# Optimization experiments

Hardware: AMD Instinct MI355X
Metric: run time of the kernel (lower is better)

## Reference

```python
import jax, jax.numpy as jnp
import numpy as np

N_NODES = 50000
N_EDGES = 800000
N_GRAPHS = 512
VOCAB = 100000
EMB = 64
HID = 128
CLASSES = 2


def setup_inputs() -> dict:
    key = jax.random.key(0)
    ks = jax.random.split(key, 12)
    x = jax.random.randint(ks[0], (N_NODES,), 0, VOCAB)
    edge_index = jax.random.randint(ks[1], (2, N_EDGES), 0, N_NODES)
    batch = jnp.sort(jax.random.randint(ks[2], (N_NODES,), 0, N_GRAPHS))
    s = lambda fan_in: 1.0 / np.sqrt(fan_in)
    emb_table = jax.random.normal(ks[3], (VOCAB, EMB), jnp.float32)
    w1_l = jax.random.uniform(ks[4], (EMB, HID), jnp.float32, -s(EMB), s(EMB))
    b1 = jnp.zeros((HID,), jnp.float32)
    w1_r = jax.random.uniform(ks[5], (EMB, HID), jnp.float32, -s(EMB), s(EMB))
    w2_l = jax.random.uniform(ks[6], (HID, HID), jnp.float32, -s(HID), s(HID))
    b2 = jnp.zeros((HID,), jnp.float32)
    w2_r = jax.random.uniform(ks[7], (HID, HID), jnp.float32, -s(HID), s(HID))
    w_out = jax.random.uniform(ks[8], (HID, CLASSES), jnp.float32, -s(HID), s(HID))
    b_out = jnp.zeros((CLASSES,), jnp.float32)
    return {"x": x, "edge_index": edge_index, "batch": batch,
            "emb_table": emb_table, "w1_l": w1_l, "b1": b1, "w1_r": w1_r,
            "w2_l": w2_l, "b2": b2, "w2_r": w2_r, "w_out": w_out, "b_out": b_out}


def _sage_conv(h, src, dst, w_l, b_l, w_r):
    # PyG SAGEConv (mean aggr): out = lin_l(mean_{j in N(i)} x_j) + lin_r(x_i)
    msg = h[src]                                              # [E, F] gather
    agg = jax.ops.segment_sum(msg, dst, num_segments=N_NODES)  # [N, F]
    deg = jax.ops.segment_sum(jnp.ones((src.shape[0],), h.dtype), dst,
                              num_segments=N_NODES)
    mean = agg / jnp.maximum(deg, 1.0)[:, None]
    return mean @ w_l + b_l + h @ w_r


def reference(x, edge_index, batch, emb_table, w1_l, b1, w1_r,
              w2_l, b2, w2_r, w_out, b_out):
    src, dst = edge_index[0], edge_index[1]
    h = emb_table[x]                                          # [N, EMB]
    h = jax.nn.relu(_sage_conv(h, src, dst, w1_l, b1, w1_r))
    # dropout is identity in eval mode
    h = jax.nn.relu(_sage_conv(h, src, dst, w2_l, b2, w2_r))
    # global mean pool over graphs
    pooled = jax.ops.segment_sum(h, batch, num_segments=N_GRAPHS)
    cnt = jax.ops.segment_sum(jnp.ones((N_NODES,), h.dtype), batch,
                              num_segments=N_GRAPHS)
    pooled = pooled / jnp.maximum(cnt, 1.0)[:, None]
    return pooled @ w_out + b_out                              # [G, CLASSES]
```

## Files before the change

kernel.cpp:

```cpp
#include <hip/hip_runtime.h>
#include <hip/hip_bf16.h>

#define N_NODES 50000
#define N_EDGES 800000
#define N_GRAPHS 512
#define EMB 64
#define HID 128

__device__ __forceinline__ unsigned f2bf(float f) {
    unsigned x = __float_as_uint(f);
    return (x + 0x7fffu + ((x >> 16) & 1u)) >> 16;
}
__device__ __forceinline__ unsigned packbf(float lo, float hi) {
    return f2bf(lo) | (f2bf(hi) << 16);
}
__device__ __forceinline__ float bf_lo(unsigned u) { return __uint_as_float(u << 16); }
__device__ __forceinline__ float bf_hi(unsigned u) { return __uint_as_float(u & 0xffff0000u); }

__global__ void k_embed_hist(const int* __restrict__ x, const float* __restrict__ emb,
                             const int* __restrict__ ei, uint2* __restrict__ h0b,
                             int* __restrict__ deg) {
    int t = blockIdx.x * 256 + threadIdx.x;
    if (t >= N_EDGES) return;
    int n = t >> 4, c4 = t & 15;
    const float4* e4 = (const float4*)emb;
    float4 v = e4[(size_t)x[n] * 16 + c4];
    uint2 b; b.x = packbf(v.x, v.y); b.y = packbf(v.z, v.w);
    h0b[(size_t)n * 16 + c4] = b;
    atomicAdd(&deg[ei[N_EDGES + t]], 1);
}

__global__ void k_scanA(const int* __restrict__ deg, int* __restrict__ rowptr,
                        int* __restrict__ bsums) {
    __shared__ int s[256];
    int t = threadIdx.x, i = blockIdx.x * 256 + t;
    int v = (i < N_NODES) ? deg[i] : 0;
    s[t] = v; __syncthreads();
    int xv = v;
    for (int off = 1; off < 256; off <<= 1) {
        int y = (t >= off) ? s[t - off] : 0;
        __syncthreads();
        xv += y; s[t] = xv;
        __syncthreads();
    }
    if (i < N_NODES) rowptr[i] = xv - v;
    if (t == 255) bsums[blockIdx.x] = xv;
}

__global__ void k_scanB(int* __restrict__ bsums, int nb) {
    __shared__ int s[256];
    int t = threadIdx.x;
    int v = (t < nb) ? bsums[t] : 0;
    s[t] = v; __syncthreads();
    int xv = v;
    for (int off = 1; off < 256; off <<= 1) {
        int y = (t >= off) ? s[t - off] : 0;
        __syncthreads();
        xv += y; s[t] = xv;
        __syncthreads();
    }
    if (t < nb) bsums[t] = xv - v;
}

__global__ void k_scanC(int* __restrict__ rowptr, int* __restrict__ wp,
                        const int* __restrict__ bsums) {
    int i = blockIdx.x * 256 + threadIdx.x;
    if (i < N_NODES) {
        int v = rowptr[i] + bsums[blockIdx.x];
        rowptr[i] = v;
        wp[i] = v;
    }
    if (i == 0) rowptr[N_NODES] = N_EDGES;
}

__global__ void k_scatter(const int* __restrict__ ei, int* __restrict__ wp,
                          int* __restrict__ nbr) {
    int e = blockIdx.x * 256 + threadIdx.x;
    if (e >= N_EDGES) return;
    int s = ei[e], d = ei[N_EDGES + e];
    int pos = atomicAdd(&wp[d], 1);
    nbr[pos] = s;
}

template <int F>
__device__ __forceinline__ void agg_tile_bf(const uint2* __restrict__ hb,
                                            const int* __restrict__ rowptr,
                                            const int* __restrict__ nbr,
                                            float* __restrict__ mean,
                                            int aggIdx, int t) {
    int wl = t >> 6;
    int l = t & 63;
    float4* m4 = (float4*)mean;

    int n, c;
    if constexpr (F == 128) { n = aggIdx * 16 + wl * 2 + (l >> 5); c = l & 31; }
    else                    { n = aggIdx * 32 + wl * 4 + (l >> 4); c = l & 15; }
    if (n >= N_NODES) return;
    constexpr int CU2 = F / 4;

    int r0 = rowptr[n], r1 = rowptr[n + 1];
    float inv = 1.0f / (float)max(r1 - r0, 1);

    float4 a[8];
    #pragma unroll
    for (int u = 0; u < 8; ++u) a[u] = make_float4(0.f, 0.f, 0.f, 0.f);

    int i = r0;
    for (; i + 7 < r1; i += 8) {
        int s0 = nbr[i + 0], s1 = nbr[i + 1], s2 = nbr[i + 2], s3 = nbr[i + 3];
        int s4 = nbr[i + 4], s5 = nbr[i + 5], s6 = nbr[i + 6], s7 = nbr[i + 7];
        uint2 v0 = hb[(size_t)s0 * CU2 + c];
        uint2 v1 = hb[(size_t)s1 * CU2 + c];
        uint2 v2 = hb[(size_t)s2 * CU2 + c];
        uint2 v3 = hb[(size_t)s3 * CU2 + c];
        uint2 v4 = hb[(size_t)s4 * CU2 + c];
        uint2 v5 = hb[(size_t)s5 * CU2 + c];
        uint2 v6 = hb[(size_t)s6 * CU2 + c];
        uint2 v7 = hb[(size_t)s7 * CU2 + c];
        a[0].x += bf_lo(v0.x); a[0].y += bf_hi(v0.x); a[0].z += bf_lo(v0.y); a[0].w += bf_hi(v0.y);
        a[1].x += bf_lo(v1.x); a[1].y += bf_hi(v1.x); a[1].z += bf_lo(v1.y); a[1].w += bf_hi(v1.y);
        a[2].x += bf_lo(v2.x); a[2].y += bf_hi(v2.x); a[2].z += bf_lo(v2.y); a[2].w += bf_hi(v2.y);
        a[3].x += bf_lo(v3.x); a[3].y += bf_hi(v3.x); a[3].z += bf_lo(v3.y); a[3].w += bf_hi(v3.y);
        a[4].x += bf_lo(v4.x); a[4].y += bf_hi(v4.x); a[4].z += bf_lo(v4.y); a[4].w += bf_hi(v4.y);
        a[5].x += bf_lo(v5.x); a[5].y += bf_hi(v5.x); a[5].z += bf_lo(v5.y); a[5].w += bf_hi(v5.y);
        a[6].x += bf_lo(v6.x); a[6].y += bf_hi(v6.x); a[6].z += bf_lo(v6.y); a[6].w += bf_hi(v6.y);
        a[7].x += bf_lo(v7.x); a[7].y += bf_hi(v7.x); a[7].z += bf_lo(v7.y); a[7].w += bf_hi(v7.y);
    }
    for (; i + 3 < r1; i += 4) {
        int s0 = nbr[i + 0], s1 = nbr[i + 1], s2 = nbr[i + 2], s3 = nbr[i + 3];
        uint2 v0 = hb[(size_t)s0 * CU2 + c];
        uint2 v1 = hb[(size_t)s1 * CU2 + c];
        uint2 v2 = hb[(size_t)s2 * CU2 + c];
        uint2 v3 = hb[(size_t)s3 * CU2 + c];
        a[0].x += bf_lo(v0.x); a[0].y += bf_hi(v0.x); a[0].z += bf_lo(v0.y); a[0].w += bf_hi(v0.y);
        a[1].x += bf_lo(v1.x); a[1].y += bf_hi(v1.x); a[1].z += bf_lo(v1.y); a[1].w += bf_hi(v1.y);
        a[2].x += bf_lo(v2.x); a[2].y += bf_hi(v2.x); a[2].z += bf_lo(v2.y); a[2].w += bf_hi(v2.y);
        a[3].x += bf_lo(v3.x); a[3].y += bf_hi(v3.x); a[3].z += bf_lo(v3.y); a[3].w += bf_hi(v3.y);
    }
    for (; i < r1; ++i) {
        uint2 v = hb[(size_t)nbr[i] * CU2 + c];
        a[0].x += bf_lo(v.x); a[0].y += bf_hi(v.x); a[0].z += bf_lo(v.y); a[0].w += bf_hi(v.y);
    }
    #pragma unroll
    for (int u = 1; u < 8; ++u) {
        a[0].x += a[u].x; a[0].y += a[u].y; a[0].z += a[u].z; a[0].w += a[u].w;
    }
    m4[(size_t)n * CU2 + c] = make_float4(a[0].x * inv, a[0].y * inv,
                                          a[0].z * inv, a[0].w * inv);
}

template <int K>
__device__ __forceinline__ void stage_f32(const float* __restrict__ hin, int base,
                                          int t, float* ls) {
    constexpr int LS = K + 2, C4 = K / 4;
    const float4* h4 = (const float4*)hin;
    for (int idx = t; idx < 64 * C4; idx += 512) {
        int r = idx / C4, c = idx % C4;
        float4 v = (base + r < N_NODES) ? h4[(size_t)(base + r) * C4 + c]
                                        : make_float4(0.f, 0.f, 0.f, 0.f);
        float* dp = &ls[r * LS + c * 4];
        dp[0] = v.x; dp[1] = v.y; dp[2] = v.z; dp[3] = v.w;
    }
}

template <int K>
__device__ __forceinline__ void stage_bf(const uint2* __restrict__ hb, int base,
                                         int t, float* ls) {
    constexpr int LS = K + 2, C2 = K / 4;
    for (int idx = t; idx < 64 * C2; idx += 512) {
        int r = idx / C2, c = idx % C2;
        uint2 v = (base + r < N_NODES) ? hb[(size_t)(base + r) * C2 + c]
                                       : make_uint2(0u, 0u);
        float* dp = &ls[r * LS + c * 4];
        dp[0] = bf_lo(v.x); dp[1] = bf_hi(v.x);
        dp[2] = bf_lo(v.y); dp[3] = bf_hi(v.y);
    }
}

template <int K>
__device__ __forceinline__ void gemm_core(const float* __restrict__ lrow,
                                          const float* __restrict__ w,
                                          int j0, float (&acc)[16]) {
    #pragma unroll 4
    for (int k = 0; k < K; ++k) {
        float hv = lrow[k];
        const float* wk = &w[(size_t)k * 128 + j0];
        #pragma unroll
        for (int j = 0; j < 16; ++j) acc[j] = fmaf(hv, wk[j], acc[j]);
    }
}

__global__ __launch_bounds__(512) void k_fuse1(
    const uint2* __restrict__ h0b, const int* __restrict__ rowptr,
    const int* __restrict__ nbr, float* __restrict__ mean1,
    const float* __restrict__ w1r, const float* __restrict__ b1,
    float* __restrict__ pre1) {
    __shared__ float ls[64 * 66];
    int b = blockIdx.x, t = threadIdx.x;
    if (b % 3 == 2) {
        int base = (b / 3) * 64;
        stage_bf<64>(h0b, base, t, ls);
        __syncthreads();
        int lane = t & 63, wid = __builtin_amdgcn_readfirstlane(t >> 6), j0 = wid * 16;
        int node = base + lane;
        float acc[16];
        #pragma unroll
        for (int j = 0; j < 16; ++j) acc[j] = b1[j0 + j];
        gemm_core<64>(&ls[lane * 66], w1r, j0, acc);
        if (node < N_NODES) {
            float4* o4 = (float4*)pre1;
            #pragma unroll
            for (int jj = 0; jj < 4; ++jj)
                o4[(size_t)node * 32 + wid * 4 + jj] =
                    make_float4(acc[jj*4], acc[jj*4+1], acc[jj*4+2], acc[jj*4+3]);
        }
    } else {
        agg_tile_bf<64>(h0b, rowptr, nbr, mean1, (b / 3) * 2 + (b % 3), t);
    }
}

__global__ __launch_bounds__(512) void k_fuse2(
    const uint2* __restrict__ h1b, const int* __restrict__ rowptr,
    const int* __restrict__ nbr, float* __restrict__ mean2,
    const float* __restrict__ w2r, const float* __restrict__ b2,
    float* __restrict__ pre2) {
    __shared__ float ls[64 * 130];
    int b = blockIdx.x, t = threadIdx.x;
    if (b % 5 == 4) {
        int base = (b / 5) * 64;
        stage_bf<128>(h1b, base, t, ls);
        __syncthreads();
        int lane = t & 63, wid = __builtin_amdgcn_readfirstlane(t >> 6), j0 = wid * 16;
        int node = base + lane;
        float acc[16];
        #pragma unroll
        for (int j = 0; j < 16; ++j) acc[j] = b2[j0 + j];
        gemm_core<128>(&ls[lane * 130], w2r, j0, acc);
        if (node < N_NODES) {
            float4* o4 = (float4*)pre2;
            #pragma unroll
            for (int jj = 0; jj < 4; ++jj)
                o4[(size_t)node * 32 + wid * 4 + jj] =
                    make_float4(acc[jj*4], acc[jj*4+1], acc[jj*4+2], acc[jj*4+3]);
        }
    } else {
        agg_tile_bf<128>(h1b, rowptr, nbr, mean2, (b / 5) * 4 + (b % 5), t);
    }
}

__global__ __launch_bounds__(512) void k_gemm_mean64(
    const float* __restrict__ mean1, const float* __restrict__ w1l,
    const float* __restrict__ pre1, uint2* __restrict__ h1b) {
    __shared__ float ls[64 * 66];
    int t = threadIdx.x, base = blockIdx.x * 64;
    stage_f32<64>(mean1, base, t, ls);
    __syncthreads();
    int lane = t & 63, wid = __builtin_amdgcn_readfirstlane(t >> 6), j0 = wid * 16;
    int node = base + lane;
    bool valid = node < N_NODES;
    float acc[16];
    const float4* p4 = (const float4*)pre1;
    #pragma unroll
    for (int jj = 0; jj < 4; ++jj) {
        float4 v = valid ? p4[(size_t)node * 32 + wid * 4 + jj]
                         : make_float4(0.f, 0.f, 0.f, 0.f);
        acc[jj*4] = v.x; acc[jj*4+1] = v.y; acc[jj*4+2] = v.z; acc[jj*4+3] = v.w;
    }
    gemm_core<64>(&ls[lane * 66], w1l, j0, acc);
    if (!valid) return;
    #pragma unroll
    for (int jj = 0; jj < 4; ++jj) {
        float a0 = fmaxf(acc[jj*4+0], 0.f), a1 = fmaxf(acc[jj*4+1], 0.f);
        float a2 = fmaxf(acc[jj*4+2], 0.f), a3 = fmaxf(acc[jj*4+3], 0.f);
        uint2 u; u.x = packbf(a0, a1); u.y = packbf(a2, a3);
        h1b[(size_t)node * 32 + wid * 4 + jj] = u;
    }
}

__global__ __launch_bounds__(512) void k_mean128_pool(
    const float* __restrict__ mean2, const float* __restrict__ w2l,
    const float* __restrict__ pre2, const int* __restrict__ batch,
    float* __restrict__ pooled) {
    __shared__ float ls[64 * 130];
    __shared__ int bb[64];
    int t = threadIdx.x, base = blockIdx.x * 64;
    stage_f32<128>(mean2, base, t, ls);
    if (t < 64) bb[t] = (base + t < N_NODES) ? batch[base + t] : -1;
    __syncthreads();
    int lane = t & 63, wid = __builtin_amdgcn_readfirstlane(t >> 6), j0 = wid * 16;
    int node = base + lane;
    bool valid = node < N_NODES;
    float acc[16];
    const float4* p4 = (const float4*)pre2;
    #pragma unroll
    for (int jj = 0; jj < 4; ++jj) {
        float4 v = valid ? p4[(size_t)node * 32 + wid * 4 + jj]
                         : make_float4(0.f, 0.f, 0.f, 0.f);
        acc[jj*4] = v.x; acc[jj*4+1] = v.y; acc[jj*4+2] = v.z; acc[jj*4+3] = v.w;
    }
    gemm_core<128>(&ls[lane * 130], w2l, j0, acc);
    __syncthreads();
    #pragma unroll
    for (int j = 0; j < 16; ++j)
        ls[lane * 129 + j0 + j] = valid ? fmaxf(acc[j], 0.f) : 0.f;
    __syncthreads();
    if (t < 128) {
        int col = t;
        float run = 0.f;
        int gcur = bb[0];
        for (int r = 0; r < 64; ++r) {
            int g = bb[r];
            if (g != gcur) {
                if (gcur >= 0) atomicAdd(&pooled[gcur * 128 + col], run);
                run = 0.f; gcur = g;
            }
            run += ls[r * 129 + col];
        }
        if (gcur >= 0) atomicAdd(&pooled[gcur * 128 + col], run);
    }
}

__global__ void k_head(const float* __restrict__ pooled, const int* __restrict__ batch,
                       const float* __restrict__ w_out, const float* __restrict__ b_out,
                       float* __restrict__ out) {
    int g = blockIdx.x, f = threadIdx.x;
    int lo = 0, hi = N_NODES;
    while (lo < hi) { int m = (lo + hi) >> 1; if (batch[m] < g) lo = m + 1; else hi = m; }
    int s = lo;
    lo = s; hi = N_NODES;
    while (lo < hi) { int m = (lo + hi) >> 1; if (batch[m] < g + 1) lo = m + 1; else hi = m; }
    int cnt = lo - s;
    float p = pooled[(size_t)g * 128 + f] / (float)max(cnt, 1);
    __shared__ float red[256];
    red[f] = p * w_out[f * 2 + 0];
    red[128 + f] = p * w_out[f * 2 + 1];
    __syncthreads();
    for (int st = 64; st > 0; st >>= 1) {
        if (f < st) { red[f] += red[f + st]; red[128 + f] += red[128 + f + st]; }
        __syncthreads();
    }
    if (f == 0) {
        out[(size_t)g * 2 + 0] = red[0] + b_out[0];
        out[(size_t)g * 2 + 1] = red[128] + b_out[1];
    }
}

extern "C" void kernel_launch(void* const* d_in, const int* in_sizes, int n_in,
                              void* d_out, int out_size, void* d_ws, size_t ws_size,
                              hipStream_t stream) {
    const int*   x      = (const int*)d_in[0];
    const int*   ei     = (const int*)d_in[1];
    const int*   batch  = (const int*)d_in[2];
    const float* emb    = (const float*)d_in[3];
    const float* w1_l   = (const float*)d_in[4];
    const float* b1     = (const float*)d_in[5];
    const float* w1_r   = (const float*)d_in[6];
    const float* w2_l   = (const float*)d_in[7];
    const float* b2     = (const float*)d_in[8];
    const float* w2_r   = (const float*)d_in[9];
    const float* w_out  = (const float*)d_in[10];
    const float* b_out  = (const float*)d_in[11];
    float* out = (float*)d_out;

    float* F = (float*)d_ws;
    float* mean1 = F;
    uint2* h1b   = (uint2*)F;
    float* pre1  = F + (size_t)N_NODES * 64;
    float* pre2  = pre1;
    float* mean2 = pre1 + (size_t)N_NODES * 128;
    uint2* h0b   = (uint2*)(mean2 + (size_t)N_NODES * 128);
    int*   deg   = (int*)((float*)h0b + (size_t)N_NODES * 32);
    float* pooled= (float*)(deg + N_NODES);
    int*   rowptr= (int*)(pooled + (size_t)N_GRAPHS * 128);
    int*   wp    = rowptr + N_NODES + 1;
    int*   nbr   = wp + N_NODES;
    int*   bsums = nbr + N_EDGES;

    const int NB = (N_NODES + 255) / 256;
    const int GB = (N_NODES + 63) / 64;

    hipMemsetAsync(deg, 0, (size_t)N_NODES * sizeof(int)
                          + (size_t)N_GRAPHS * 128 * sizeof(float), stream);

    k_embed_hist<<<(N_EDGES + 255) / 256, 256, 0, stream>>>(x, emb, ei, h0b, deg);
    k_scanA<<<NB, 256, 0, stream>>>(deg, rowptr, bsums);
    k_scanB<<<1, 256, 0, stream>>>(bsums, NB);
    k_scanC<<<NB, 256, 0, stream>>>(rowptr, wp, bsums);
    k_scatter<<<(N_EDGES + 255) / 256, 256, 0, stream>>>(ei, wp, nbr);

    k_fuse1<<<3 * GB, 512, 0, stream>>>(h0b, rowptr, nbr, mean1, w1_r, b1, pre1);
    k_gemm_mean64<<<GB, 512, 0, stream>>>(mean1, w1_l, pre1, h1b);

    k_fuse2<<<5 * GB, 512, 0, stream>>>(h1b, rowptr, nbr, mean2, w2_r, b2, pre2);
    k_mean128_pool<<<GB, 512, 0, stream>>>(mean2, w2_l, pre2, batch, pooled);

    k_head<<<N_GRAPHS, 128, 0, stream>>>(pooled, batch, w_out, b_out, out);

    (void)in_sizes; (void)n_in; (void)out_size; (void)ws_size;
}
```

Measured before the change: 332.8 us.

## Fuse neighbor aggregation and both linear transforms into one kernel per layer

Each SAGE layer now runs as a single kernel per 64-node tile. The kernel aggregates the neighbor mean straight into LDS, stages the self features as packed bf16, and computes both matmuls plus ReLU (and pooling for layer 2) without writing mean or pre-activation arrays to global memory. This removes two kernel launches and the fp32 global round-trips of mean1/mean2/pre1/pre2. The trade-off is fewer, heavier blocks with more LDS per block, where gather latency and GEMM are now serialized within a block instead of spread over separate blocks, which may reduce parallelism and latency hiding.

```diff
diff --git a/kernel.cpp b/kernel.cpp
--- a/kernel.cpp
+++ b/kernel.cpp
@@ -4,8 +4,6 @@
 #define N_NODES 50000
 #define N_EDGES 800000
 #define N_GRAPHS 512
-#define EMB 64
-#define HID 128
 
 __device__ __forceinline__ unsigned f2bf(float f) {
     unsigned x = __float_as_uint(f);
@@ -83,227 +81,175 @@
 }
 
 template <int F>
-__device__ __forceinline__ void agg_tile_bf(const uint2* __restrict__ hb,
-                                            const int* __restrict__ rowptr,
-                                            const int* __restrict__ nbr,
-                                            float* __restrict__ mean,
-                                            int aggIdx, int t) {
-    int wl = t >> 6;
-    int l = t & 63;
-    float4* m4 = (float4*)mean;
-
-    int n, c;
-    if constexpr (F == 128) { n = aggIdx * 16 + wl * 2 + (l >> 5); c = l & 31; }
-    else                    { n = aggIdx * 32 + wl * 4 + (l >> 4); c = l & 15; }
-    if (n >= N_NODES) return;
+__device__ __forceinline__ void agg_to_lds(const uint2* __restrict__ hb,
+                                           const int* __restrict__ rowptr,
+                                           const int* __restrict__ nbr,
+                                           int base, int pass, int t,
+                                           float* __restrict__ tB) {
     constexpr int CU2 = F / 4;
-
-    int r0 = rowptr[n], r1 = rowptr[n + 1];
-    float inv = 1.0f / (float)max(r1 - r0, 1);
-
-    float4 a[8];
-    #pragma unroll
-    for (int u = 0; u < 8; ++u) a[u] = make_float4(0.f, 0.f, 0.f, 0.f);
-
-    int i = r0;
-    for (; i + 7 < r1; i += 8) {
-        int s0 = nbr[i + 0], s1 = nbr[i + 1], s2 = nbr[i + 2], s3 = nbr[i + 3];
-        int s4 = nbr[i + 4], s5 = nbr[i + 5], s6 = nbr[i + 6], s7 = nbr[i + 7];
-        uint2 v0 = hb[(size_t)s0 * CU2 + c];
-        uint2 v1 = hb[(size_t)s1 * CU2 + c];
-        uint2 v2 = hb[(size_t)s2 * CU2 + c];
-        uint2 v3 = hb[(size_t)s3 * CU2 + c];
-        uint2 v4 = hb[(size_t)s4 * CU2 + c];
-        uint2 v5 = hb[(size_t)s5 * CU2 + c];
-        uint2 v6 = hb[(size_t)s6 * CU2 + c];
-        uint2 v7 = hb[(size_t)s7 * CU2 + c];
-        a[0].x += bf_lo(v0.x); a[0].y += bf_hi(v0.x); a[0].z += bf_lo(v0.y); a[0].w += bf_hi(v0.y);
-        a[1].x += bf_lo(v1.x); a[1].y += bf_hi(v1.x); a[1].z += bf_lo(v1.y); a[1].w += bf_hi(v1.y);
-        a[2].x += bf_lo(v2.x); a[2].y += bf_hi(v2.x); a[2].z += bf_lo(v2.y); a[2].w += bf_hi(v2.y);
-        a[3].x += bf_lo(v3.x); a[3].y += bf_hi(v3.x); a[3].z += bf_lo(v3.y); a[3].w += bf_hi(v3.y);
-        a[4].x += bf_lo(v4.x); a[4].y += bf_hi(v4.x); a[4].z += bf_lo(v4.y); a[4].w += bf_hi(v4.y);
-        a[5].x += bf_lo(v5.x); a[5].y += bf_hi(v5.x); a[5].z += bf_lo(v5.y); a[5].w += bf_hi(v5.y);
-        a[6].x += bf_lo(v6.x); a[6].y += bf_hi(v6.x); a[6].z += bf_lo(v6.y); a[6].w += bf_hi(v6.y);
-        a[7].x += bf_lo(v7.x); a[7].y += bf_hi(v7.x); a[7].z += bf_lo(v7.y); a[7].w += bf_hi(v7.y);
-    }
-    for (; i + 3 < r1; i += 4) {
-        int s0 = nbr[i + 0], s1 = nbr[i + 1], s2 = nbr[i + 2], s3 = nbr[i + 3];
-        uint2 v0 = hb[(size_t)s0 * CU2 + c];
-        uint2 v1 = hb[(size_t)s1 * CU2 + c];
-        uint2 v2 = hb[(size_t)s2 * CU2 + c];
-        uint2 v3 = hb[(size_t)s3 * CU2 + c];
-        a[0].x += bf_lo(v0.x); a[0].y += bf_hi(v0.x); a[0].z += bf_lo(v0.y); a[0].w += bf_hi(v0.y);
-        a[1].x += bf_lo(v1.x); a[1].y += bf_hi(v1.x); a[1].z += bf_lo(v1.y); a[1].w += bf_hi(v1.y);
-        a[2].x += bf_lo(v2.x); a[2].y += bf_hi(v2.x); a[2].z += bf_lo(v2.y); a[2].w += bf_hi(v2.y);
-        a[3].x += bf_lo(v3.x); a[3].y += bf_hi(v3.x); a[3].z += bf_lo(v3.y); a[3].w += bf_hi(v3.y);
-    }
-    for (; i < r1; ++i) {
-        uint2 v = hb[(size_t)nbr[i] * CU2 + c];
-        a[0].x += bf_lo(v.x); a[0].y += bf_hi(v.x); a[0].z += bf_lo(v.y); a[0].w += bf_hi(v.y);
-    }
-    #pragma unroll
-    for (int u = 1; u < 8; ++u) {
-        a[0].x += a[u].x; a[0].y += a[u].y; a[0].z += a[u].z; a[0].w += a[u].w;
-    }
-    m4[(size_t)n * CU2 + c] = make_float4(a[0].x * inv, a[0].y * inv,
-                                          a[0].z * inv, a[0].w * inv);
+    constexpr int NPW = 64 / CU2;
+    constexpr int LSB = F + 2;
+    int wl = t >> 6, l = t & 63;
+    int nIT = pass * (8 * NPW) + wl * NPW + (l / CU2);
+    int c = l & (CU2 - 1);
+    int n = base + nIT;
+    if (n < N_NODES) {
+        int r0 = rowptr[n], r1 = rowptr[n + 1];
+        float inv = 1.0f / (float)max(r1 - r0, 1);
+        float4 a[8];
+        #pragma unroll
+        for (int u = 0; u < 8; ++u) a[u] = make_float4(0.f, 0.f, 0.f, 0.f);
+        int i = r0;
+        for (; i + 7 < r1; i += 8) {
+            int s0 = nbr[i + 0], s1 = nbr[i + 1], s2 = nbr[i + 2], s3 = nbr[i + 3];
+            int s4 = nbr[i + 4], s5 = nbr[i + 5], s6 = nbr[i + 6], s7 = nbr[i + 7];
+            uint2 v0 = hb[(size_t)s0 * CU2 + c];
+            uint2 v1 = hb[(size_t)s1 * CU2 + c];
+            uint2 v2 = hb[(size_t)s2 * CU2 + c];
+            uint2 v3 = hb[(size_t)s3 * CU2 + c];
+            uint2 v4 = hb[(size_t)s4 * CU2 + c];
+            uint2 v5 = hb[(size_t)s5 * CU2 + c];
+            uint2 v6 = hb[(size_t)s6 * CU2 + c];
+            uint2 v7 = hb[(size_t)s7 * CU2 + c];
+            a[0].x += bf_lo(v0.x); a[0].y += bf_hi(v0.x); a[0].z += bf_lo(v0.y); a[0].w += bf_hi(v0.y);
+            a[1].x += bf_lo(v1.x); a[1].y += bf_hi(v1.x); a[1].z += bf_lo(v1.y); a[1].w += bf_hi(v1.y);
+            a[2].x += bf_lo(v2.x); a[2].y += bf_hi(v2.x); a[2].z += bf_lo(v2.y); a[2].w += bf_hi(v2.y);
+            a[3].x += bf_lo(v3.x); a[3].y += bf_hi(v3.x); a[3].z += bf_lo(v3.y); a[3].w += bf_hi(v3.y);
+            a[4].x += bf_lo(v4.x); a[4].y += bf_hi(v4.x); a[4].z += bf_lo(v4.y); a[4].w += bf_hi(v4.y);
+            a[5].x += bf_lo(v5.x); a[5].y += bf_hi(v5.x); a[5].z += bf_lo(v5.y); a[5].w += bf_hi(v5.y);
+            a[6].x += bf_lo(v6.x); a[6].y += bf_hi(v6.x); a[6].z += bf_lo(v6.y); a[6].w += bf_hi(v6.y);
+            a[7].x += bf_lo(v7.x); a[7].y += bf_hi(v7.x); a[7].z += bf_lo(v7.y); a[7].w += bf_hi(v7.y);
+        }
+        for (; i + 3 < r1; i += 4) {
+            int s0 = nbr[i + 0], s1 = nbr[i + 1], s2 = nbr[i + 2], s3 = nbr[i + 3];
+            uint2 v0 = hb[(size_t)s0 * CU2 + c];
+            uint2 v1 = hb[(size_t)s1 * CU2 + c];
+            uint2 v2 = hb[(size_t)s2 * CU2 + c];
+            uint2 v3 = hb[(size_t)s3 * CU2 + c];
+            a[0].x += bf_lo(v0.x); a[0].y += bf_hi(v0.x); a[0].z += bf_lo(v0.y); a[0].w += bf_hi(v0.y);
+            a[1].x += bf_lo(v1.x); a[1].y += bf_hi(v1.x); a[1].z += bf_lo(v1.y); a[1].w += bf_hi(v1.y);
+            a[2].x += bf_lo(v2.x); a[2].y += bf_hi(v2.x); a[2].z += bf_lo(v2.y); a[2].w += bf_hi(v2.y);
+            a[3].x += bf_lo(v3.x); a[3].y += bf_hi(v3.x); a[3].z += bf_lo(v3.y); a[3].w += bf_hi(v3.y);
+        }
+        for (; i < r1; ++i) {
+            uint2 v = hb[(size_t)nbr[i] * CU2 + c];
+            a[0].x += bf_lo(v.x); a[0].y += bf_hi(v.x); a[0].z += bf_lo(v.y); a[0].w += bf_hi(v.y);
+        }
+        #pragma unroll
+        for (int u = 1; u < 8; ++u) {
+            a[0].x += a[u].x; a[0].y += a[u].y; a[0].z += a[u].z; a[0].w += a[u].w;
+        }
+        float* dp = &tB[nIT * LSB + c * 4];
+        dp[0] = a[0].x * inv; dp[1] = a[0].y * inv;
+        dp[2] = a[0].z * inv; dp[3] = a[0].w * inv;
+    }
 }
 
 template <int K>
-__device__ __forceinline__ void stage_f32(const float* __restrict__ hin, int base,
-                                          int t, float* ls) {
-    constexpr int LS = K + 2, C4 = K / 4;
-    const float4* h4 = (const float4*)hin;
-    for (int idx = t; idx < 64 * C4; idx += 512) {
-        int r = idx / C4, c = idx % C4;
-        float4 v = (base + r < N_NODES) ? h4[(size_t)(base + r) * C4 + c]
-                                        : make_float4(0.f, 0.f, 0.f, 0.f);
-        float* dp = &ls[r * LS + c * 4];
-        dp[0] = v.x; dp[1] = v.y; dp[2] = v.z; dp[3] = v.w;
+__device__ __forceinline__ void gemm_bf_core(const unsigned* __restrict__ rowA,
+                                             const float* __restrict__ w,
+                                             int j0, float (&acc)[16]) {
+    #pragma unroll 2
+    for (int k2 = 0; k2 < K / 2; ++k2) {
+        unsigned u = rowA[k2];
+        float hv0 = bf_lo(u), hv1 = bf_hi(u);
+        const float* w0 = &w[(size_t)(2 * k2) * 128 + j0];
+        const float* w1 = &w[(size_t)(2 * k2 + 1) * 128 + j0];
+        #pragma unroll
+        for (int j = 0; j < 16; ++j) acc[j] = fmaf(hv0, w0[j], acc[j]);
+        #pragma unroll
+        for (int j = 0; j < 16; ++j) acc[j] = fmaf(hv1, w1[j], acc[j]);
     }
 }
 
 template <int K>
-__device__ __forceinline__ void stage_bf(const uint2* __restrict__ hb, int base,
-                                         int t, float* ls) {
-    constexpr int LS = K + 2, C2 = K / 4;
-    for (int idx = t; idx < 64 * C2; idx += 512) {
-        int r = idx / C2, c = idx % C2;
-        uint2 v = (base + r < N_NODES) ? hb[(size_t)(base + r) * C2 + c]
-                                       : make_uint2(0u, 0u);
-        float* dp = &ls[r * LS + c * 4];
-        dp[0] = bf_lo(v.x); dp[1] = bf_hi(v.x);
-        dp[2] = bf_lo(v.y); dp[3] = bf_hi(v.y);
-    }
-}
-
-template <int K>
-__device__ __forceinline__ void gemm_core(const float* __restrict__ lrow,
-                                          const float* __restrict__ w,
-                                          int j0, float (&acc)[16]) {
+__device__ __forceinline__ void gemm_f32_core(const float* __restrict__ rowB,
+                                              const float* __restrict__ w,
+                                              int j0, float (&acc)[16]) {
     #pragma unroll 4
     for (int k = 0; k < K; ++k) {
-        float hv = lrow[k];
+        float hv = rowB[k];
         const float* wk = &w[(size_t)k * 128 + j0];
         #pragma unroll
         for (int j = 0; j < 16; ++j) acc[j] = fmaf(hv, wk[j], acc[j]);
     }
 }
 
-__global__ __launch_bounds__(512) void k_fuse1(
+__global__ __launch_bounds__(512) void k_layer1(
     const uint2* __restrict__ h0b, const int* __restrict__ rowptr,
-    const int* __restrict__ nbr, float* __restrict__ mean1,
-    const float* __restrict__ w1r, const float* __restrict__ b1,
-    float* __restrict__ pre1) {
-    __shared__ float ls[64 * 66];
-    int b = blockIdx.x, t = threadIdx.x;
-    if (b % 3 == 2) {
-        int base = (b / 3) * 64;
-        stage_bf<64>(h0b, base, t, ls);
-        __syncthreads();
-        int lane = t & 63, wid = __builtin_amdgcn_readfirstlane(t >> 6), j0 = wid * 16;
-        int node = base + lane;
-        float acc[16];
-        #pragma unroll
-        for (int j = 0; j < 16; ++j) acc[j] = b1[j0 + j];
-        gemm_core<64>(&ls[lane * 66], w1r, j0, acc);
-        if (node < N_NODES) {
-            float4* o4 = (float4*)pre1;
-            #pragma unroll
-            for (int jj = 0; jj < 4; ++jj)
-                o4[(size_t)node * 32 + wid * 4 + jj] =
-                    make_float4(acc[jj*4], acc[jj*4+1], acc[jj*4+2], acc[jj*4+3]);
-        }
-    } else {
-        agg_tile_bf<64>(h0b, rowptr, nbr, mean1, (b / 3) * 2 + (b % 3), t);
-    }
-}
-
-__global__ __launch_bounds__(512) void k_fuse2(
+    const int* __restrict__ nbr, const float* __restrict__ w1r,
+    const float* __restrict__ w1l, const float* __restrict__ b1,
+    uint2* __restrict__ h1b) {
+    __shared__ unsigned tA[64 * 33];
+    __shared__ float tB[64 * 66];
+    int t = threadIdx.x, base = blockIdx.x * 64;
+
+    for (int idx = t; idx < 1024; idx += 512) {
+        int r = idx >> 4, c = idx & 15;
+        uint2 v = (base + r < N_NODES) ? h0b[(size_t)(base + r) * 16 + c]
+                                       : make_uint2(0u, 0u);
+        tA[r * 33 + c * 2] = v.x; tA[r * 33 + c * 2 + 1] = v.y;
+    }
+    agg_to_lds<64>(h0b, rowptr, nbr, base, 0, t, tB);
+    agg_to_lds<64>(h0b, rowptr, nbr, base, 1, t, tB);
+    __syncthreads();
+
+    int lane = t & 63, wid = __builtin_amdgcn_readfirstlane(t >> 6), j0 = wid * 16;
+    int node = base + lane;
+    float acc[16];
+    #pragma unroll
+    for (int j = 0; j < 16; ++j) acc[j] = b1[j0 + j];
+    gemm_bf_core<64>(&tA[lane * 33], w1r, j0, acc);
+    gemm_f32_core<64>(&tB[lane * 66], w1l, j0, acc);
+
+    if (node < N_NODES) {
+        #pragma unroll
+        for (int jj = 0; jj < 4; ++jj) {
+            float a0 = fmaxf(acc[jj * 4 + 0], 0.f), a1 = fmaxf(acc[jj * 4 + 1], 0.f);
+            float a2 = fmaxf(acc[jj * 4 + 2], 0.f), a3 = fmaxf(acc[jj * 4 + 3], 0.f);
+            uint2 u; u.x = packbf(a0, a1); u.y = packbf(a2, a3);
+            h1b[(size_t)node * 32 + wid * 4 + jj] = u;
+        }
+    }
+}
+
+__global__ __launch_bounds__(512) void k_layer2_pool(
     const uint2* __restrict__ h1b, const int* __restrict__ rowptr,
-    const int* __restrict__ nbr, float* __restrict__ mean2,
-    const float* __restrict__ w2r, const float* __restrict__ b2,
-    float* __restrict__ pre2) {
-    __shared__ float ls[64 * 130];
-    int b = blockIdx.x, t = threadIdx.x;
-    if (b % 5 == 4) {
-        int base = (b / 5) * 64;
-        stage_bf<128>(h1b, base, t, ls);
-        __syncthreads();
-        int lane = t & 63, wid = __builtin_amdgcn_readfirstlane(t >> 6), j0 = wid * 16;
-        int node = base + lane;
-        float acc[16];
-        #pragma unroll
-        for (int j = 0; j < 16; ++j) acc[j] = b2[j0 + j];
-        gemm_core<128>(&ls[lane * 130], w2r, j0, acc);
-        if (node < N_NODES) {
-            float4* o4 = (float4*)pre2;
-            #pragma unroll
-            for (int jj = 0; jj < 4; ++jj)
-                o4[(size_t)node * 32 + wid * 4 + jj] =
-                    make_float4(acc[jj*4], acc[jj*4+1], acc[jj*4+2], acc[jj*4+3]);
-        }
-    } else {
-        agg_tile_bf<128>(h1b, rowptr, nbr, mean2, (b / 5) * 4 + (b % 5), t);
-    }
-}
-
-__global__ __launch_bounds__(512) void k_gemm_mean64(
-    const float* __restrict__ mean1, const float* __restrict__ w1l,
-    const float* __restrict__ pre1, uint2* __restrict__ h1b) {
-    __shared__ float ls[64 * 66];
+    const int* __restrict__ nbr, const float* __restrict__ w2r,
+    const float* __restrict__ w2l, const float* __restrict__ b2,
+    const int* __restrict__ batch, float* __restrict__ pooled) {
+    __shared__ unsigned tA[64 * 65];
+    __shared__ float tB[64 * 130];
+    __shared__ int bb[64];
     int t = threadIdx.x, base = blockIdx.x * 64;
-    stage_f32<64>(mean1, base, t, ls);
-    __syncthreads();
+
+    for (int idx = t; idx < 2048; idx += 512) {
+        int r = idx >> 5, c = idx & 31;
+        uint2 v = (base + r < N_NODES) ? h1b[(size_t)(base + r) * 32 + c]
+                                       : make_uint2(0u, 0u);
+        tA[r * 65 + c * 2] = v.x; tA[r * 65 + c * 2 + 1] = v.y;
+    }
+    if (t < 64) bb[t] = (base + t < N_NODES) ? batch[base + t] : -1;
+    #pragma unroll 1
+    for (int pass = 0; pass < 4; ++pass)
+        agg_to_lds<128>(h1b, rowptr, nbr, base, pass, t, tB);
+    __syncthreads();
+
     int lane = t & 63, wid = __builtin_amdgcn_readfirstlane(t >> 6), j0 = wid * 16;
     int node = base + lane;
     bool valid = node < N_NODES;
     float acc[16];
-    const float4* p4 = (const float4*)pre1;
     #pragma unroll
-    for (int jj = 0; jj < 4; ++jj) {
-        float4 v = valid ? p4[(size_t)node * 32 + wid * 4 + jj]
-                         : make_float4(0.f, 0.f, 0.f, 0.f);
-        acc[jj*4] = v.x; acc[jj*4+1] = v.y; acc[jj*4+2] = v.z; acc[jj*4+3] = v.w;
-    }
-    gemm_core<64>(&ls[lane * 66], w1l, j0, acc);
-    if (!valid) return;
-    #pragma unroll
-    for (int jj = 0; jj < 4; ++jj) {
-        float a0 = fmaxf(acc[jj*4+0], 0.f), a1 = fmaxf(acc[jj*4+1], 0.f);
-        float a2 = fmaxf(acc[jj*4+2], 0.f), a3 = fmaxf(acc[jj*4+3], 0.f);
-        uint2 u; u.x = packbf(a0, a1); u.y = packbf(a2, a3);
-        h1b[(size_t)node * 32 + wid * 4 + jj] = u;
-    }
-}
-
-__global__ __launch_bounds__(512) void k_mean128_pool(
-    const float* __restrict__ mean2, const float* __restrict__ w2l,
-    const float* __restrict__ pre2, const int* __restrict__ batch,
-    float* __restrict__ pooled) {
-    __shared__ float ls[64 * 130];
-    __shared__ int bb[64];
-    int t = threadIdx.x, base = blockIdx.x * 64;
-    stage_f32<128>(mean2, base, t, ls);
-    if (t < 64) bb[t] = (base + t < N_NODES) ? batch[base + t] : -1;
-    __syncthreads();
-    int lane = t & 63, wid = __builtin_amdgcn_readfirstlane(t >> 6), j0 = wid * 16;
-    int node = base + lane;
-    bool valid = node < N_NODES;
-    float acc[16];
-    const float4* p4 = (const float4*)pre2;
-    #pragma unroll
-    for (int jj = 0; jj < 4; ++jj) {
-        float4 v = valid ? p4[(size_t)node * 32 + wid * 4 + jj]
-                         : make_float4(0.f, 0.f, 0.f, 0.f);
-        acc[jj*4] = v.x; acc[jj*4+1] = v.y; acc[jj*4+2] = v.z; acc[jj*4+3] = v.w;
-    }
-    gemm_core<128>(&ls[lane * 130], w2l, j0, acc);
-    __syncthreads();
+    for (int j = 0; j < 16; ++j) acc[j] = b2[j0 + j];
+    gemm_bf_core<128>(&tA[lane * 65], w2r, j0, acc);
+    gemm_f32_core<128>(&tB[lane * 130], w2l, j0, acc);
+    __syncthreads();
+
     #pragma unroll
     for (int j = 0; j < 16; ++j)
-        ls[lane * 129 + j0 + j] = valid ? fmaxf(acc[j], 0.f) : 0.f;
-    __syncthreads();
+        tB[lane * 129 + j0 + j] = valid ? fmaxf(acc[j], 0.f) : 0.f;
+    __syncthreads();
+
     if (t < 128) {
         int col = t;
         float run = 0.f;
@@ -314,7 +260,7 @@
                 if (gcur >= 0) atomicAdd(&pooled[gcur * 128 + col], run);
                 run = 0.f; gcur = g;
             }
-            run += ls[r * 129 + col];
+            run += tB[r * 129 + col];
         }
         if (gcur >= 0) atomicAdd(&pooled[gcur * 128 + col], run);
     }
@@ -362,14 +308,9 @@
     const float* b_out  = (const float*)d_in[11];
     float* out = (float*)d_out;
 
-    float* F = (float*)d_ws;
-    float* mean1 = F;
-    uint2* h1b   = (uint2*)F;
-    float* pre1  = F + (size_t)N_NODES * 64;
-    float* pre2  = pre1;
-    float* mean2 = pre1 + (size_t)N_NODES * 128;
-    uint2* h0b   = (uint2*)(mean2 + (size_t)N_NODES * 128);
-    int*   deg   = (int*)((float*)h0b + (size_t)N_NODES * 32);
+    uint2* h0b   = (uint2*)d_ws;
+    uint2* h1b   = h0b + (size_t)N_NODES * 16;
+    int*   deg   = (int*)(h1b + (size_t)N_NODES * 32);
     float* pooled= (float*)(deg + N_NODES);
     int*   rowptr= (int*)(pooled + (size_t)N_GRAPHS * 128);
     int*   wp    = rowptr + N_NODES + 1;
@@ -388,12 +329,9 @@
     k_scanC<<<NB, 256, 0, stream>>>(rowptr, wp, bsums);
     k_scatter<<<(N_EDGES + 255) / 256, 256, 0, stream>>>(ei, wp, nbr);
 
-    k_fuse1<<<3 * GB, 512, 0, stream>>>(h0b, rowptr, nbr, mean1, w1_r, b1, pre1);
-    k_gemm_mean64<<<GB, 512, 0, stream>>>(mean1, w1_l, pre1, h1b);
-
-    k_fuse2<<<5 * GB, 512, 0, stream>>>(h1b, rowptr, nbr, mean2, w2_r, b2, pre2);
-    k_mean128_pool<<<GB, 512, 0, stream>>>(mean2, w2_l, pre2, batch, pooled);
-
+    k_layer1<<<GB, 512, 0, stream>>>(h0b, rowptr, nbr, w1_r, w1_l, b1, h1b);
+    k_layer2_pool<<<GB, 512, 0, stream>>>(h1b, rowptr, nbr, w2_r, w2_l, b2,
+                                          batch, pooled);
     k_head<<<N_GRAPHS, 128, 0, stream>>>(pooled, batch, w_out, b_out, out);
 
     (void)in_sizes; (void)n_in; (void)out_size; (void)ws_size;
```

Result: no change. 331.8 us (-0.3%).
